# Kernel optimization log

Measured on AMD Instinct MI355X. Metric: run time of the kernel, lower is better.

## Reference

```python
import jax, jax.numpy as jnp
import numpy as np

# ---- config matching init_kwargs ----
B, D, U = 8192, 1024, 512
F, E, T = 4, 4, 2
MAX_VAL = 10000000000.0
MIN_VAL = -10000000000.0
DISC_IDX = np.array([[0, 1, 2, 3], [4, 5, 6, 7]])  # discrete fields 0,1: per-expert feature index
CONT_IDX = np.array([8, 9])                         # continuous fields 2,3: single feature index
BOUNDS = np.array([-0.5, 0.0, 0.5])                 # 3 boundaries -> 4 buckets per continuous field
LOWERS = np.concatenate([[MIN_VAL], BOUNDS]).astype(np.float32)
UPPERS = np.concatenate([BOUNDS, [MAX_VAL]]).astype(np.float32)


def setup_inputs() -> dict:
    key = jax.random.key(0)
    ks = jax.random.split(key, 8)
    s_in = 1.0 / np.sqrt(D)
    s_cat = 1.0 / np.sqrt(2 * U)
    x = jax.random.normal(ks[0], (B, D), dtype=jnp.float32)
    Wc = jax.random.normal(ks[1], (D, U), dtype=jnp.float32) * s_in      # common expert kernel
    bc = jnp.zeros((U,), dtype=jnp.float32)
    We = jax.random.normal(ks[2], (F, E, D, U), dtype=jnp.float32) * s_in  # per-field per-expert kernels
    be = jnp.zeros((F, E, U), dtype=jnp.float32)
    Wg = jax.random.normal(ks[3], (T, D, F + 1), dtype=jnp.float32) * s_in  # per-task gate kernels
    bg = jnp.zeros((T, F + 1), dtype=jnp.float32)
    Wa = jax.random.normal(ks[4], (F, 2 * U, 1), dtype=jnp.float32) * s_cat  # attention kernels
    ba = jnp.zeros((F, 1), dtype=jnp.float32)
    Wu = jax.random.normal(ks[5], (F, 2 * U, 1), dtype=jnp.float32) * s_cat  # update kernels
    bu = jnp.zeros((F, 1), dtype=jnp.float32)
    return {"x": x, "Wc": Wc, "bc": bc, "We": We, "be": be,
            "Wg": Wg, "bg": bg, "Wa": Wa, "ba": ba, "Wu": Wu, "bu": bu}


def _field_masks(x):
    # discrete fields: expert j active iff x[:, idx[i][j]] > 0
    m_disc = x[:, DISC_IDX] > 0.0                         # [B, 2, E]
    # continuous fields: bucket x[:, idx] by boundaries (lower < v <= upper)
    v = x[:, CONT_IDX][..., None]                         # [B, 2, 1]
    m_cont = (v > LOWERS) & (v <= UPPERS)                 # [B, 2, E]
    return jnp.concatenate([m_disc, m_cont], axis=1).astype(x.dtype)  # [B, F, E]


def reference(x, Wc, bc, We, be, Wg, bg, Wa, ba, Wu, bu):
    # common expert: [B, U]
    common = jax.nn.relu(x @ Wc + bc)
    # all field experts at once: [B, F, E, U]
    e = jax.nn.relu(jnp.einsum('bd,fedu->bfeu', x, We) + be)
    mask = _field_masks(x)                                # [B, F, E]
    # mask-select active expert(s) per field: [B, F, U]
    field_out = jnp.einsum('bfe,bfeu->bfu', mask, e)
    # concat [common, field] per field: [B, F, 2U]
    cat = jnp.concatenate(
        [jnp.broadcast_to(common[:, None, :], field_out.shape), field_out], axis=-1)
    # sigmoid attention reweights field expert output
    att = jax.nn.sigmoid(jnp.einsum('bfk,fko->bfo', cat, Wa) + ba[None])   # [B, F, 1]
    field_att = att * field_out
    # sigmoid update gate blends field expert with common expert
    upd = jax.nn.sigmoid(jnp.einsum('bfk,fko->bfo', cat, Wu) + bu[None])   # [B, F, 1]
    field_final = upd * field_att + (1.0 - upd) * common[:, None, :]       # [B, F, U]
    # experts = [common] + per-field outputs: [B, F+1, U]
    experts = jnp.concatenate([common[:, None, :], field_final], axis=1)
    # per-task softmax gates over F+1 experts: [B, T, F+1]
    gates = jax.nn.softmax(jnp.einsum('bd,tdg->btg', x, Wg) + bg[None], axis=-1)
    # task outputs: [B, T, U]
    return jnp.einsum('btg,bgu->btu', gates, experts)
```

## Files before the change

### kernel.cpp

```cpp
#include <hip/hip_runtime.h>

typedef unsigned short ushort_t;

#define B_SZ 8192
#define D_SZ 1024
#define U_SZ 512
#define F_SZ 4
#define E_SZ 4
#define T_SZ 2

typedef __attribute__((ext_vector_type(8))) short bf16x8;
typedef __attribute__((ext_vector_type(4))) float f32x4;
typedef __attribute__((ext_vector_type(8))) unsigned short u16x8;

__device__ __forceinline__ unsigned short f2bf(float f) {
  union { float f; unsigned int u; } v; v.f = f;
  unsigned int r = v.u + 0x7FFFu + ((v.u >> 16) & 1u);
  return (unsigned short)(r >> 16);
}
__device__ __forceinline__ float bf2f(unsigned short h) {
  union { unsigned int u; float f; } v; v.u = ((unsigned int)h) << 16;
  return v.f;
}

__device__ __forceinline__ void gload_lds16(const void* g, void* l) {
  __builtin_amdgcn_global_load_lds(
      (const __attribute__((address_space(1))) unsigned int*)g,
      (__attribute__((address_space(3))) unsigned int*)l, 16, 0, 0);
}

__global__ __launch_bounds__(256) void conv_x(const float* __restrict__ x,
                                              ushort_t* __restrict__ xbf) {
  const size_t i = ((size_t)blockIdx.x * 256 + threadIdx.x) * 8;
  const float4 a = *(const float4*)(x + i);
  const float4 c = *(const float4*)(x + i + 4);
  u16x8 o;
  o[0] = f2bf(a.x); o[1] = f2bf(a.y); o[2] = f2bf(a.z); o[3] = f2bf(a.w);
  o[4] = f2bf(c.x); o[5] = f2bf(c.y); o[6] = f2bf(c.z); o[7] = f2bf(c.w);
  *(u16x8*)(xbf + i) = o;
}

__global__ __launch_bounds__(256) void conv_w(const float* __restrict__ Wc,
                                              const float* __restrict__ We,
                                              ushort_t* __restrict__ wbf) {
  const int blk = blockIdx.x;
  const int midx = blk >> 9;
  const int tid = blk & 511;
  const int trow = (tid >> 4) * 32;
  const int tcol = (tid & 15) * 32;
  const float* src = (midx == 0) ? Wc : (We + (size_t)(midx - 1) * D_SZ * U_SZ);
  ushort_t* dst = wbf + (size_t)midx * U_SZ * D_SZ;
  __shared__ float tile[32][33];
  const int c = threadIdx.x & 31;
  const int r = threadIdx.x >> 5;
#pragma unroll
  for (int k = 0; k < 4; ++k)
    tile[r + k * 8][c] = src[(size_t)(trow + r + k * 8) * U_SZ + tcol + c];
  __syncthreads();
#pragma unroll
  for (int k = 0; k < 4; ++k) {
    const int rr = r + k * 8;
    dst[(size_t)(tcol + rr) * D_SZ + trow + c] = f2bf(tile[c][rr]);
  }
}

__global__ __launch_bounds__(256) void mask_k(const float* __restrict__ x,
                                              float* __restrict__ mask) {
  const int b = blockIdx.x * 256 + threadIdx.x;
  const float* xr = x + (size_t)b * D_SZ;
  float m[16];
#pragma unroll
  for (int f = 0; f < 2; ++f)
#pragma unroll
    for (int j = 0; j < 4; ++j)
      m[f * 4 + j] = (xr[f * 4 + j] > 0.f) ? 1.f : 0.f;
  const float LO[4] = {-1e10f, -0.5f, 0.f, 0.5f};
  const float HI[4] = {-0.5f, 0.f, 0.5f, 1e10f};
#pragma unroll
  for (int f = 0; f < 2; ++f) {
    const float v = xr[8 + f];
#pragma unroll
    for (int j = 0; j < 4; ++j)
      m[8 + f * 4 + j] = ((v > LO[j]) && (v <= HI[j])) ? 1.f : 0.f;
  }
#pragma unroll
  for (int k = 0; k < 4; ++k) {
    float4 v4 = {m[k * 4], m[k * 4 + 1], m[k * 4 + 2], m[k * 4 + 3]};
    *(float4*)(mask + (size_t)b * 16 + k * 4) = v4;
  }
}

__global__ __launch_bounds__(256) void gates_k(const float* __restrict__ x,
                                               const float* __restrict__ Wg,
                                               const float* __restrict__ bg,
                                               float* __restrict__ gates) {
  const int t = threadIdx.x;
  const int lane = t & 63;
  const int w = t >> 6;
  const int b = blockIdx.x * 4 + w;
  const float* xr = x + (size_t)b * D_SZ;
  float p[10];
#pragma unroll
  for (int j = 0; j < 10; ++j) p[j] = 0.f;
#pragma unroll
  for (int i = 0; i < 4; ++i) {
    const int d0 = i * 256 + lane * 4;
    const float4 xv = *(const float4*)(xr + d0);
#pragma unroll
    for (int t2 = 0; t2 < 2; ++t2) {
      const float* wg = Wg + t2 * (D_SZ * 5) + d0 * 5;
#pragma unroll
      for (int g = 0; g < 5; ++g)
        p[t2 * 5 + g] += xv.x * wg[g] + xv.y * wg[5 + g] + xv.z * wg[10 + g] + xv.w * wg[15 + g];
    }
  }
#pragma unroll
  for (int off = 32; off > 0; off >>= 1)
#pragma unroll
    for (int j = 0; j < 10; ++j) p[j] += __shfl_xor(p[j], off);
  float l[10];
#pragma unroll
  for (int j = 0; j < 10; ++j) l[j] = p[j] + bg[j];
  const float mx0 = fmaxf(fmaxf(fmaxf(l[0], l[1]), fmaxf(l[2], l[3])), l[4]);
  const float mx1 = fmaxf(fmaxf(fmaxf(l[5], l[6]), fmaxf(l[7], l[8])), l[9]);
  float ev[10]; float s0 = 0.f, s1 = 0.f;
#pragma unroll
  for (int g = 0; g < 5; ++g) { ev[g] = expf(l[g] - mx0); s0 += ev[g]; }
#pragma unroll
  for (int g = 5; g < 10; ++g) { ev[g] = expf(l[g] - mx1); s1 += ev[g]; }
  if (lane < 5) gates[(size_t)b * 10 + lane] = ev[lane] / s0;
  else if (lane < 10) gates[(size_t)b * 10 + lane] = ev[lane] / s1;
}

__global__ __launch_bounds__(256, 2) void gemm_fused(
    const ushort_t* __restrict__ xbf, const ushort_t* __restrict__ wbf,
    const float* __restrict__ mask, const float* __restrict__ bc,
    const float* __restrict__ be,
    ushort_t* __restrict__ common, ushort_t* __restrict__ fout) {
  __shared__ ushort_t Ash[128 * 64];
  __shared__ ushort_t Bsh[128 * 64];
  __shared__ float mk[128 * 4];

  const int t = threadIdx.x;
  const int lane = t & 63;
  const int w = t >> 6;
  const int wm = w >> 1;
  const int wn = w & 1;
  const int quad = lane >> 4;
  const int l16 = lane & 15;
  const int m0 = blockIdx.x * 128;
  const int grp = blockIdx.y;
  const bool isCommon = grp >= 16;
  const int f = isCommon ? 0 : (grp >> 2);
  const int uc = isCommon ? (grp - 16) : (grp & 3);
  const int u0 = uc * 128;
  const int nExp = isCommon ? 1 : 4;
  const int midx0 = isCommon ? 0 : (1 + f * 4);

  if (!isCommon && t < 128)
    *(float4*)(&mk[t * 4]) = *(const float4*)(mask + (size_t)(m0 + t) * 16 + f * 4);

  int offs[4];
#pragma unroll
  for (int i = 0; i < 4; ++i) {
    const int c = (w * 4 + i) * 64 + lane;
    const int r = c >> 3;
    const int gc = (c & 7) ^ (r & 7);
    offs[i] = r * D_SZ + gc * 8;
  }
  const ushort_t* xbase = xbf + (size_t)m0 * D_SZ;

  int rowA[4], rowB[4];
#pragma unroll
  for (int i = 0; i < 4; ++i) {
    rowA[i] = wm * 64 + i * 16 + l16;
    rowB[i] = wn * 64 + i * 16 + l16;
  }
  int sw[2];
  sw[0] = ((quad) ^ (l16 & 7)) * 8;
  sw[1] = ((4 + quad) ^ (l16 & 7)) * 8;

  const f32x4 fzero = {0.f, 0.f, 0.f, 0.f};
  f32x4 facc[4][4];
#pragma unroll
  for (int mi = 0; mi < 4; ++mi)
#pragma unroll
    for (int ni = 0; ni < 4; ++ni) facc[mi][ni] = fzero;

  for (int e = 0; e < nExp; ++e) {
    const ushort_t* wbase = wbf + (size_t)(midx0 + e) * (U_SZ * D_SZ) + (size_t)u0 * D_SZ;
    f32x4 acc[4][4];
#pragma unroll
    for (int mi = 0; mi < 4; ++mi)
#pragma unroll
      for (int ni = 0; ni < 4; ++ni) acc[mi][ni] = fzero;

    for (int k0 = 0; k0 < D_SZ; k0 += 64) {
#pragma unroll
      for (int i = 0; i < 4; ++i) {
        gload_lds16(xbase + offs[i] + k0, (char*)Ash + (w * 4 + i) * 1024);
        gload_lds16(wbase + offs[i] + k0, (char*)Bsh + (w * 4 + i) * 1024);
      }
      __syncthreads();
#pragma unroll
      for (int qs = 0; qs < 2; ++qs) {
        bf16x8 av[4], bv[4];
#pragma unroll
        for (int mi = 0; mi < 4; ++mi)
          av[mi] = *(const bf16x8*)(Ash + rowA[mi] * 64 + sw[qs]);
#pragma unroll
        for (int ni = 0; ni < 4; ++ni)
          bv[ni] = *(const bf16x8*)(Bsh + rowB[ni] * 64 + sw[qs]);
#pragma unroll
        for (int mi = 0; mi < 4; ++mi)
#pragma unroll
          for (int ni = 0; ni < 4; ++ni)
            acc[mi][ni] = __builtin_amdgcn_mfma_f32_16x16x32_bf16(av[mi], bv[ni],
                                                                  acc[mi][ni], 0, 0, 0);
      }
      __syncthreads();
    }

    if (isCommon) {
#pragma unroll
      for (int mi = 0; mi < 4; ++mi) {
        const int rowb = m0 + wm * 64 + mi * 16 + quad * 4;
#pragma unroll
        for (int ni = 0; ni < 4; ++ni) {
          const int u = u0 + wn * 64 + ni * 16 + l16;
          const float bcv = bc[u];
#pragma unroll
          for (int r = 0; r < 4; ++r) {
            const float v = fmaxf(acc[mi][ni][r] + bcv, 0.f);
            common[(size_t)(rowb + r) * U_SZ + u] = f2bf(v);
          }
        }
      }
    } else {
#pragma unroll
      for (int ni = 0; ni < 4; ++ni) {
        const int u = u0 + wn * 64 + ni * 16 + l16;
        const float bev = be[(f * 4 + e) * U_SZ + u];
#pragma unroll
        for (int mi = 0; mi < 4; ++mi) {
          const int rowl = wm * 64 + mi * 16 + quad * 4;
#pragma unroll
          for (int r = 0; r < 4; ++r) {
            const float mval = mk[(rowl + r) * 4 + e];
            const float v = fmaxf(acc[mi][ni][r] + bev, 0.f);
            facc[mi][ni][r] += mval * v;
          }
        }
      }
    }
  }

  if (!isCommon) {
#pragma unroll
    for (int mi = 0; mi < 4; ++mi) {
      const int rowl = wm * 64 + mi * 16 + quad * 4;
#pragma unroll
      for (int ni = 0; ni < 4; ++ni) {
        const int u = u0 + wn * 64 + ni * 16 + l16;
#pragma unroll
        for (int r = 0; r < 4; ++r)
          fout[((size_t)(m0 + rowl + r) * F_SZ + f) * U_SZ + u] = f2bf(facc[mi][ni][r]);
      }
    }
  }
}

__global__ __launch_bounds__(256) void stage2_k(
    const ushort_t* __restrict__ common, const ushort_t* __restrict__ fout,
    const float* __restrict__ gates,
    const float* __restrict__ Wa, const float* __restrict__ ba,
    const float* __restrict__ Wu, const float* __restrict__ bu,
    float* __restrict__ out) {
  const int b = blockIdx.x;
  const int t = threadIdx.x;
  const int lane = t & 63;
  const int w = t >> 6;

  const float c0 = bf2f(common[(size_t)b * U_SZ + t]);
  const float c1 = bf2f(common[(size_t)b * U_SZ + 256 + t]);
  float fo0[4], fo1[4];
#pragma unroll
  for (int f = 0; f < 4; ++f) {
    fo0[f] = bf2f(fout[((size_t)b * F_SZ + f) * U_SZ + t]);
    fo1[f] = bf2f(fout[((size_t)b * F_SZ + f) * U_SZ + 256 + t]);
  }
  float pa[4], pu[4];
#pragma unroll
  for (int f = 0; f < 4; ++f) {
    const float* wa = Wa + f * 1024;
    pa[f] = c0 * wa[t] + c1 * wa[256 + t] + fo0[f] * wa[512 + t] + fo1[f] * wa[768 + t];
    const float* wu = Wu + f * 1024;
    pu[f] = c0 * wu[t] + c1 * wu[256 + t] + fo0[f] * wu[512 + t] + fo1[f] * wu[768 + t];
  }
#pragma unroll
  for (int off = 32; off > 0; off >>= 1) {
#pragma unroll
    for (int f = 0; f < 4; ++f) {
      pa[f] += __shfl_xor(pa[f], off);
      pu[f] += __shfl_xor(pu[f], off);
    }
  }
  __shared__ float redA[4][4];
  __shared__ float redU[4][4];
  __shared__ float gsh[10];
  if (lane == 0) {
#pragma unroll
    for (int f = 0; f < 4; ++f) { redA[w][f] = pa[f]; redU[w][f] = pu[f]; }
  }
  if (t < 10) gsh[t] = gates[(size_t)b * 10 + t];
  __syncthreads();
  float att[4], upd[4], ff0[4], ff1[4];
#pragma unroll
  for (int f = 0; f < 4; ++f) {
    const float sa = redA[0][f] + redA[1][f] + redA[2][f] + redA[3][f] + ba[f];
    const float su = redU[0][f] + redU[1][f] + redU[2][f] + redU[3][f] + bu[f];
    att[f] = 1.f / (1.f + expf(-sa));
    upd[f] = 1.f / (1.f + expf(-su));
    ff0[f] = upd[f] * (att[f] * fo0[f]) + (1.f - upd[f]) * c0;
    ff1[f] = upd[f] * (att[f] * fo1[f]) + (1.f - upd[f]) * c1;
  }
#pragma unroll
  for (int t2 = 0; t2 < 2; ++t2) {
    float v0 = gsh[t2 * 5] * c0;
    float v1 = gsh[t2 * 5] * c1;
#pragma unroll
    for (int f = 0; f < 4; ++f) {
      v0 += gsh[t2 * 5 + 1 + f] * ff0[f];
      v1 += gsh[t2 * 5 + 1 + f] * ff1[f];
    }
    out[((size_t)b * T_SZ + t2) * U_SZ + t] = v0;
    out[((size_t)b * T_SZ + t2) * U_SZ + 256 + t] = v1;
  }
}

extern "C" void kernel_launch(void* const* d_in, const int* in_sizes, int n_in,
                              void* d_out, int out_size, void* d_ws, size_t ws_size,
                              hipStream_t stream) {
  (void)in_sizes; (void)n_in; (void)out_size; (void)ws_size;
  const float* x  = (const float*)d_in[0];
  const float* Wc = (const float*)d_in[1];
  const float* bc = (const float*)d_in[2];
  const float* We = (const float*)d_in[3];
  const float* be = (const float*)d_in[4];
  const float* Wg = (const float*)d_in[5];
  const float* bg = (const float*)d_in[6];
  const float* Wa = (const float*)d_in[7];
  const float* ba = (const float*)d_in[8];
  const float* Wu = (const float*)d_in[9];
  const float* bu = (const float*)d_in[10];
  float* out = (float*)d_out;
  char* ws = (char*)d_ws;

  const size_t O_XBF    = 0;
  const size_t O_WBF    = O_XBF + (size_t)B_SZ * D_SZ * 2;
  const size_t O_MASK   = O_WBF + (size_t)17 * U_SZ * D_SZ * 2;
  const size_t O_GATES  = O_MASK + (size_t)B_SZ * 16 * 4;
  const size_t O_COMMON = O_GATES + (size_t)B_SZ * 10 * 4;
  const size_t O_FOUT   = O_COMMON + (size_t)B_SZ * U_SZ * 2;

  ushort_t* xbf    = (ushort_t*)(ws + O_XBF);
  ushort_t* wbf    = (ushort_t*)(ws + O_WBF);
  float*    maskp  = (float*)(ws + O_MASK);
  float*    gatesp = (float*)(ws + O_GATES);
  ushort_t* commonp= (ushort_t*)(ws + O_COMMON);
  ushort_t* foutp  = (ushort_t*)(ws + O_FOUT);

  conv_x<<<dim3(4096), dim3(256), 0, stream>>>(x, xbf);
  conv_w<<<dim3(17 * 512), dim3(256), 0, stream>>>(Wc, We, wbf);
  mask_k<<<dim3(32), dim3(256), 0, stream>>>(x, maskp);
  gates_k<<<dim3(2048), dim3(256), 0, stream>>>(x, Wg, bg, gatesp);
  gemm_fused<<<dim3(64, 20), dim3(256), 0, stream>>>(xbf, wbf, maskp, bc, be, commonp, foutp);
  stage2_k<<<dim3(8192), dim3(256), 0, stream>>>(commonp, foutp, gatesp, Wa, ba, Wu, bu, out);
}
```

Measured before the change: 332.6 us.

## Fuse mask into conv_x, widen conv_w transpose tiles, stage gate weights in LDS

Computes the field masks inside the x-to-bf16 conversion kernel, which removes one launch and a second read of x. The weight transpose now uses 64x64 tiles with float4 loads and 16-byte bf16 stores instead of scalar accesses. The gate kernel transposes Wg into shared memory and processes two rows per wave, so it reads weights with vector LDS loads instead of strided global loads. The cost is extra LDS use and a per-block staging pass over Wg.

```diff
diff --git a/kernel.cpp b/kernel.cpp
--- a/kernel.cpp
+++ b/kernel.cpp
@@ -30,7 +30,8 @@
 }
 
 __global__ __launch_bounds__(256) void conv_x(const float* __restrict__ x,
-                                              ushort_t* __restrict__ xbf) {
+                                              ushort_t* __restrict__ xbf,
+                                              float* __restrict__ mask) {
   const size_t i = ((size_t)blockIdx.x * 256 + threadIdx.x) * 8;
   const float4 a = *(const float4*)(x + i);
   const float4 c = *(const float4*)(x + i + 4);
@@ -38,55 +39,63 @@
   o[0] = f2bf(a.x); o[1] = f2bf(a.y); o[2] = f2bf(a.z); o[3] = f2bf(a.w);
   o[4] = f2bf(c.x); o[5] = f2bf(c.y); o[6] = f2bf(c.z); o[7] = f2bf(c.w);
   *(u16x8*)(xbf + i) = o;
+
+  if ((threadIdx.x & 127) == 0) {
+    const int b = blockIdx.x * 2 + (threadIdx.x >> 7);
+    const float* xr = x + (size_t)b * D_SZ;
+    float m[16];
+    m[0] = a.x > 0.f ? 1.f : 0.f; m[1] = a.y > 0.f ? 1.f : 0.f;
+    m[2] = a.z > 0.f ? 1.f : 0.f; m[3] = a.w > 0.f ? 1.f : 0.f;
+    m[4] = c.x > 0.f ? 1.f : 0.f; m[5] = c.y > 0.f ? 1.f : 0.f;
+    m[6] = c.z > 0.f ? 1.f : 0.f; m[7] = c.w > 0.f ? 1.f : 0.f;
+    const float LO[4] = {-1e10f, -0.5f, 0.f, 0.5f};
+    const float HI[4] = {-0.5f, 0.f, 0.5f, 1e10f};
+    const float v0 = xr[8], v1 = xr[9];
+#pragma unroll
+    for (int j = 0; j < 4; ++j) {
+      m[8 + j]  = ((v0 > LO[j]) && (v0 <= HI[j])) ? 1.f : 0.f;
+      m[12 + j] = ((v1 > LO[j]) && (v1 <= HI[j])) ? 1.f : 0.f;
+    }
+#pragma unroll
+    for (int k = 0; k < 4; ++k) {
+      float4 v4 = {m[k * 4], m[k * 4 + 1], m[k * 4 + 2], m[k * 4 + 3]};
+      *(float4*)(mask + (size_t)b * 16 + k * 4) = v4;
+    }
+  }
 }
 
 __global__ __launch_bounds__(256) void conv_w(const float* __restrict__ Wc,
                                               const float* __restrict__ We,
                                               ushort_t* __restrict__ wbf) {
   const int blk = blockIdx.x;
-  const int midx = blk >> 9;
-  const int tid = blk & 511;
-  const int trow = (tid >> 4) * 32;
-  const int tcol = (tid & 15) * 32;
+  const int midx = blk >> 7;
+  const int tid = blk & 127;
+  const int trow = (tid >> 3) * 64;
+  const int tcol = (tid & 7) * 64;
   const float* src = (midx == 0) ? Wc : (We + (size_t)(midx - 1) * D_SZ * U_SZ);
   ushort_t* dst = wbf + (size_t)midx * U_SZ * D_SZ;
-  __shared__ float tile[32][33];
-  const int c = threadIdx.x & 31;
-  const int r = threadIdx.x >> 5;
-#pragma unroll
-  for (int k = 0; k < 4; ++k)
-    tile[r + k * 8][c] = src[(size_t)(trow + r + k * 8) * U_SZ + tcol + c];
+
+  __shared__ float tile[64][69];
+  const int t = threadIdx.x;
+  const int r0 = t >> 2;
+  const int cseg = (t & 3) * 16;
+#pragma unroll
+  for (int j = 0; j < 4; ++j) {
+    const float4 v = *(const float4*)(src + (size_t)(trow + r0) * U_SZ + tcol + cseg + j * 4);
+    tile[r0][cseg + j * 4 + 0] = v.x;
+    tile[r0][cseg + j * 4 + 1] = v.y;
+    tile[r0][cseg + j * 4 + 2] = v.z;
+    tile[r0][cseg + j * 4 + 3] = v.w;
+  }
   __syncthreads();
-#pragma unroll
-  for (int k = 0; k < 4; ++k) {
-    const int rr = r + k * 8;
-    dst[(size_t)(tcol + rr) * D_SZ + trow + c] = f2bf(tile[c][rr]);
-  }
-}
-
-__global__ __launch_bounds__(256) void mask_k(const float* __restrict__ x,
-                                              float* __restrict__ mask) {
-  const int b = blockIdx.x * 256 + threadIdx.x;
-  const float* xr = x + (size_t)b * D_SZ;
-  float m[16];
-#pragma unroll
-  for (int f = 0; f < 2; ++f)
-#pragma unroll
-    for (int j = 0; j < 4; ++j)
-      m[f * 4 + j] = (xr[f * 4 + j] > 0.f) ? 1.f : 0.f;
-  const float LO[4] = {-1e10f, -0.5f, 0.f, 0.5f};
-  const float HI[4] = {-0.5f, 0.f, 0.5f, 1e10f};
-#pragma unroll
-  for (int f = 0; f < 2; ++f) {
-    const float v = xr[8 + f];
-#pragma unroll
-    for (int j = 0; j < 4; ++j)
-      m[8 + f * 4 + j] = ((v > LO[j]) && (v <= HI[j])) ? 1.f : 0.f;
-  }
-#pragma unroll
-  for (int k = 0; k < 4; ++k) {
-    float4 v4 = {m[k * 4], m[k * 4 + 1], m[k * 4 + 2], m[k * 4 + 3]};
-    *(float4*)(mask + (size_t)b * 16 + k * 4) = v4;
+  const int u = t >> 2;
+  const int d0 = (t & 3) * 16;
+#pragma unroll
+  for (int h = 0; h < 2; ++h) {
+    u16x8 ov;
+#pragma unroll
+    for (int k = 0; k < 8; ++k) ov[k] = f2bf(tile[d0 + h * 8 + k][u]);
+    *(u16x8*)(dst + (size_t)(tcol + u) * D_SZ + trow + d0 + h * 8) = ov;
   }
 }
 
@@ -94,42 +103,54 @@
                                                const float* __restrict__ Wg,
                                                const float* __restrict__ bg,
                                                float* __restrict__ gates) {
+  __shared__ float wgT[10 * 1024];
   const int t = threadIdx.x;
+#pragma unroll
+  for (int j = 0; j < 40; ++j) {
+    const int i = j * 256 + t;
+    const int t2 = i / 5120;
+    const int rem = i - t2 * 5120;
+    const int d = rem / 5;
+    const int g = rem - d * 5;
+    wgT[(t2 * 5 + g) * 1024 + d] = Wg[i];
+  }
+  __syncthreads();
   const int lane = t & 63;
   const int w = t >> 6;
-  const int b = blockIdx.x * 4 + w;
-  const float* xr = x + (size_t)b * D_SZ;
-  float p[10];
-#pragma unroll
-  for (int j = 0; j < 10; ++j) p[j] = 0.f;
-#pragma unroll
-  for (int i = 0; i < 4; ++i) {
-    const int d0 = i * 256 + lane * 4;
-    const float4 xv = *(const float4*)(xr + d0);
-#pragma unroll
-    for (int t2 = 0; t2 < 2; ++t2) {
-      const float* wg = Wg + t2 * (D_SZ * 5) + d0 * 5;
-#pragma unroll
-      for (int g = 0; g < 5; ++g)
-        p[t2 * 5 + g] += xv.x * wg[g] + xv.y * wg[5 + g] + xv.z * wg[10 + g] + xv.w * wg[15 + g];
-    }
-  }
-#pragma unroll
-  for (int off = 32; off > 0; off >>= 1)
-#pragma unroll
-    for (int j = 0; j < 10; ++j) p[j] += __shfl_xor(p[j], off);
-  float l[10];
-#pragma unroll
-  for (int j = 0; j < 10; ++j) l[j] = p[j] + bg[j];
-  const float mx0 = fmaxf(fmaxf(fmaxf(l[0], l[1]), fmaxf(l[2], l[3])), l[4]);
-  const float mx1 = fmaxf(fmaxf(fmaxf(l[5], l[6]), fmaxf(l[7], l[8])), l[9]);
-  float ev[10]; float s0 = 0.f, s1 = 0.f;
-#pragma unroll
-  for (int g = 0; g < 5; ++g) { ev[g] = expf(l[g] - mx0); s0 += ev[g]; }
-#pragma unroll
-  for (int g = 5; g < 10; ++g) { ev[g] = expf(l[g] - mx1); s1 += ev[g]; }
-  if (lane < 5) gates[(size_t)b * 10 + lane] = ev[lane] / s0;
-  else if (lane < 10) gates[(size_t)b * 10 + lane] = ev[lane] / s1;
+#pragma unroll
+  for (int rr = 0; rr < 2; ++rr) {
+    const int b = blockIdx.x * 8 + w * 2 + rr;
+    const float* xr = x + (size_t)b * D_SZ;
+    float p[10];
+#pragma unroll
+    for (int j = 0; j < 10; ++j) p[j] = 0.f;
+#pragma unroll
+    for (int i = 0; i < 4; ++i) {
+      const int d0 = i * 256 + lane * 4;
+      const float4 xv = *(const float4*)(xr + d0);
+#pragma unroll
+      for (int g = 0; g < 10; ++g) {
+        const float4 wv = *(const float4*)(wgT + g * 1024 + d0);
+        p[g] += xv.x * wv.x + xv.y * wv.y + xv.z * wv.z + xv.w * wv.w;
+      }
+    }
+#pragma unroll
+    for (int off = 32; off > 0; off >>= 1)
+#pragma unroll
+      for (int j = 0; j < 10; ++j) p[j] += __shfl_xor(p[j], off);
+    float l[10];
+#pragma unroll
+    for (int j = 0; j < 10; ++j) l[j] = p[j] + bg[j];
+    const float mx0 = fmaxf(fmaxf(fmaxf(l[0], l[1]), fmaxf(l[2], l[3])), l[4]);
+    const float mx1 = fmaxf(fmaxf(fmaxf(l[5], l[6]), fmaxf(l[7], l[8])), l[9]);
+    float ev[10]; float s0 = 0.f, s1 = 0.f;
+#pragma unroll
+    for (int g = 0; g < 5; ++g) { ev[g] = expf(l[g] - mx0); s0 += ev[g]; }
+#pragma unroll
+    for (int g = 5; g < 10; ++g) { ev[g] = expf(l[g] - mx1); s1 += ev[g]; }
+    if (lane < 5) gates[(size_t)b * 10 + lane] = ev[lane] / s0;
+    else if (lane < 10) gates[(size_t)b * 10 + lane] = ev[lane] / s1;
+  }
 }
 
 __global__ __launch_bounds__(256, 2) void gemm_fused(
@@ -370,10 +391,9 @@
   ushort_t* commonp= (ushort_t*)(ws + O_COMMON);
   ushort_t* foutp  = (ushort_t*)(ws + O_FOUT);
 
-  conv_x<<<dim3(4096), dim3(256), 0, stream>>>(x, xbf);
-  conv_w<<<dim3(17 * 512), dim3(256), 0, stream>>>(Wc, We, wbf);
-  mask_k<<<dim3(32), dim3(256), 0, stream>>>(x, maskp);
-  gates_k<<<dim3(2048), dim3(256), 0, stream>>>(x, Wg, bg, gatesp);
+  conv_x<<<dim3(4096), dim3(256), 0, stream>>>(x, xbf, maskp);
+  conv_w<<<dim3(17 * 128), dim3(256), 0, stream>>>(Wc, We, wbf);
+  gates_k<<<dim3(1024), dim3(256), 0, stream>>>(x, Wg, bg, gatesp);
   gemm_fused<<<dim3(64, 20), dim3(256), 0, stream>>>(xbf, wbf, maskp, bc, be, commonp, foutp);
   stage2_k<<<dim3(8192), dim3(256), 0, stream>>>(commonp, foutp, gatesp, Wa, ba, Wu, bu, out);
 }
```

New measurement: 328.4 us. About the same (-1.2%).
